# Optimization experiments

Hardware: AMD Instinct MI355X
Metric: run time of the kernel (lower is better)

The kernel has to match this reference:

```python
import jax, jax.numpy as jnp
import numpy as np

H = 4096
IN = 512
OUT = 64


def setup_inputs() -> dict:
    key = jax.random.key(0)
    ks = jax.random.split(key, 10)
    return {
        "inp": jax.random.normal(ks[0], (1, IN), jnp.float32),
        "hidden": jax.random.normal(ks[1], (1, H), jnp.float32),
        "hebb": jax.random.normal(ks[2], (H, H), jnp.float32) * 0.01,
        "W_i2h": jax.random.normal(ks[3], (H, IN), jnp.float32) * (1.0 / np.sqrt(IN)),
        "b_i2h": jax.random.normal(ks[4], (H,), jnp.float32),
        "w": jax.random.uniform(ks[5], (H, H), jnp.float32) * 0.01,
        "plas": jax.random.uniform(ks[6], (H, H), jnp.float32) * 0.01,
        "learn": jnp.full((1,), 0.01, jnp.float32),
        "W_h2o": jax.random.normal(ks[7], (OUT, H), jnp.float32) * (1.0 / np.sqrt(H)),
        "b_h2o": jax.random.normal(ks[8], (OUT,), jnp.float32),
    }


def reference(inp, hidden, hebb, W_i2h, b_i2h, w, plas, learn, W_h2o, b_h2o):
    # plastic-Miconi, rule='hebb', activ='relu'
    # x = relu(i2h(input) + hidden @ (w + plas * hebb))   [1, H]
    pre = inp @ W_i2h.T + b_i2h + hidden @ (w + plas * hebb)
    x = jax.nn.relu(pre)
    # hebb <- (1 - learn) * hebb + learn * outer(hidden, x)   [H, H]
    hebb_new = (1.0 - learn) * hebb + learn * (hidden.T @ x)
    # output = tanh(h2o(x))   [1, OUT]
    out = jnp.tanh(x @ W_h2o.T + b_h2o)
    return out, x, hebb_new
```

## Files before the change

kernel.cpp:

```cpp
#include <hip/hip_runtime.h>
#include <math.h>

#define H 4096
#define INP 512
#define OUTN 64
#define H4 (H / 4)
#define SPLITS 512
#define RPS (H / SPLITS)

typedef float fx4 __attribute__((ext_vector_type(4)));

__global__ __launch_bounds__(256) void k_partial(
    const float* __restrict__ hidden,
    const float* __restrict__ w,
    const float* __restrict__ plas,
    const float* __restrict__ hebb,
    float* __restrict__ partial)
{
    const int col4 = blockIdx.x * 256 + threadIdx.x;
    const int i0   = blockIdx.y * RPS;
    const fx4* __restrict__ w4 = (const fx4*)w;
    const fx4* __restrict__ p4 = (const fx4*)plas;
    const fx4* __restrict__ h4 = (const fx4*)hebb;

    fx4 acc = (fx4)(0.f);
    size_t idx = (size_t)i0 * H4 + col4;
#pragma unroll
    for (int r = 0; r < RPS; r += 2) {
        const float hv0 = hidden[i0 + r];
        const float hv1 = hidden[i0 + r + 1];
        const fx4 wv0 = __builtin_nontemporal_load(w4 + idx);
        const fx4 pv0 = __builtin_nontemporal_load(p4 + idx);
        const fx4 hb0 = h4[idx];
        const fx4 wv1 = __builtin_nontemporal_load(w4 + idx + H4);
        const fx4 pv1 = __builtin_nontemporal_load(p4 + idx + H4);
        const fx4 hb1 = h4[idx + H4];
        acc += hv0 * (wv0 + pv0 * hb0) + hv1 * (wv1 + pv1 * hb1);
        idx += 2 * (size_t)H4;
    }
    ((fx4*)partial)[(size_t)blockIdx.y * H4 + col4] = acc;
}

__global__ __launch_bounds__(256) void k_reduce_x(
    const float* __restrict__ partial,
    const float* __restrict__ inp,
    const float* __restrict__ W_i2h,
    const float* __restrict__ b_i2h,
    float* __restrict__ x_out)
{
    const int jl  = threadIdx.x & 31;
    const int grp = threadIdx.x >> 5;
    const int j   = blockIdx.x * 32 + jl;

    float sum = 0.f;
    const float* __restrict__ p = partial + (size_t)grp * 64 * H + j;
#pragma unroll 8
    for (int s = 0; s < 64; ++s)
        sum += p[(size_t)s * H];

    const fx4* __restrict__ row4 = (const fx4*)(W_i2h + (size_t)j * INP);
    const fx4* __restrict__ in4  = (const fx4*)inp;
#pragma unroll
    for (int c = 0; c < 16; ++c) {
        const fx4 a = row4[grp * 16 + c];
        const fx4 b = in4[grp * 16 + c];
        sum += a.x * b.x + a.y * b.y + a.z * b.z + a.w * b.w;
    }

    __shared__ float red[8][32];
    red[grp][jl] = sum;
    __syncthreads();
    if (threadIdx.x < 32) {
        float t = 0.f;
#pragma unroll
        for (int g = 0; g < 8; ++g) t += red[g][jl];
        const float pre = t + b_i2h[j];
        x_out[j] = pre > 0.f ? pre : 0.f;
    }
}

__global__ __launch_bounds__(256) void k_hebb(
    const float* __restrict__ hebb,
    const float* __restrict__ hidden,
    const float* __restrict__ x,
    const float* __restrict__ learn,
    float* __restrict__ hebb_out)
{
    const int i = blockIdx.x;
    const float lr   = learn[0];
    const float om   = 1.f - lr;
    const float coef = lr * hidden[i];
    const fx4* __restrict__ hb4 = (const fx4*)hebb + (size_t)i * H4;
    const fx4* __restrict__ xx4 = (const fx4*)x;
    fx4* __restrict__ o4 = (fx4*)hebb_out + (size_t)i * H4;

    const int t = threadIdx.x;
    const fx4 a0 = hb4[t];
    const fx4 a1 = hb4[t + 256];
    const fx4 a2 = hb4[t + 512];
    const fx4 a3 = hb4[t + 768];
    const fx4 x0 = xx4[t];
    const fx4 x1 = xx4[t + 256];
    const fx4 x2 = xx4[t + 512];
    const fx4 x3 = xx4[t + 768];
    __builtin_nontemporal_store(om * a0 + coef * x0, o4 + t);
    __builtin_nontemporal_store(om * a1 + coef * x1, o4 + t + 256);
    __builtin_nontemporal_store(om * a2 + coef * x2, o4 + t + 512);
    __builtin_nontemporal_store(om * a3 + coef * x3, o4 + t + 768);
}

__global__ __launch_bounds__(256) void k_out(
    const float* __restrict__ x,
    const float* __restrict__ W_h2o,
    const float* __restrict__ b_h2o,
    float* __restrict__ out)
{
    const int o = blockIdx.x;
    const fx4* __restrict__ row4 = (const fx4*)(W_h2o + (size_t)o * H);
    const fx4* __restrict__ x4   = (const fx4*)x;
    float sum = 0.f;
#pragma unroll
    for (int c = threadIdx.x; c < H4; c += 256) {
        const fx4 a = row4[c];
        const fx4 b = x4[c];
        sum += a.x * b.x + a.y * b.y + a.z * b.z + a.w * b.w;
    }
#pragma unroll
    for (int off = 32; off > 0; off >>= 1)
        sum += __shfl_down(sum, off, 64);
    __shared__ float red[4];
    const int lane = threadIdx.x & 63;
    const int wave = threadIdx.x >> 6;
    if (lane == 0) red[wave] = sum;
    __syncthreads();
    if (threadIdx.x == 0) {
        const float s = red[0] + red[1] + red[2] + red[3];
        out[o] = tanhf(s + b_h2o[o]);
    }
}

extern "C" void kernel_launch(void* const* d_in, const int* in_sizes, int n_in,
                              void* d_out, int out_size, void* d_ws, size_t ws_size,
                              hipStream_t stream)
{
    const float* inp    = (const float*)d_in[0];
    const float* hidden = (const float*)d_in[1];
    const float* hebb   = (const float*)d_in[2];
    const float* W_i2h  = (const float*)d_in[3];
    const float* b_i2h  = (const float*)d_in[4];
    const float* w      = (const float*)d_in[5];
    const float* plas   = (const float*)d_in[6];
    const float* learn  = (const float*)d_in[7];
    const float* W_h2o  = (const float*)d_in[8];
    const float* b_h2o  = (const float*)d_in[9];

    float* out      = (float*)d_out;
    float* x        = out + OUTN;
    float* hebb_out = x + H;

    const size_t part_bytes = (size_t)SPLITS * H * sizeof(float);
    float* partial = (ws_size >= part_bytes) ? (float*)d_ws : hebb_out;

    k_partial<<<dim3(H4 / 256, SPLITS), 256, 0, stream>>>(hidden, w, plas, hebb, partial);
    k_reduce_x<<<H / 32, 256, 0, stream>>>(partial, inp, W_i2h, b_i2h, x);
    k_hebb<<<H, 256, 0, stream>>>(hebb, hidden, x, learn, hebb_out);
    k_out<<<OUTN, 256, 0, stream>>>(x, W_h2o, b_h2o, out);
}
```

Before: 245.8 us.

## Batch partial-sum loads, widen reduce block, fuse hebb update with output kernel

k_partial now issues all eight rows of hebb, w and plas loads up front before the FMA chain, which raises memory-level parallelism at the cost of more registers. k_reduce_x uses 1024-thread blocks (32 groups) so each thread reduces fewer partials, with a padded shared array. The hebb update and the h2o output kernels are merged into one launch, removing a kernel boundary, and the hebb read in the update is made nontemporal.

```diff
diff --git a/kernel.cpp b/kernel.cpp
--- a/kernel.cpp
+++ b/kernel.cpp
@@ -22,26 +22,28 @@
     const fx4* __restrict__ w4 = (const fx4*)w;
     const fx4* __restrict__ p4 = (const fx4*)plas;
     const fx4* __restrict__ h4 = (const fx4*)hebb;
+    const size_t base = (size_t)i0 * H4 + col4;
+
+    fx4 hb[RPS], wv[RPS], pv[RPS];
+#pragma unroll
+    for (int r = 0; r < RPS; ++r)
+        hb[r] = h4[base + (size_t)r * H4];
+#pragma unroll
+    for (int r = 0; r < RPS; ++r)
+        wv[r] = __builtin_nontemporal_load(w4 + base + (size_t)r * H4);
+#pragma unroll
+    for (int r = 0; r < RPS; ++r)
+        pv[r] = __builtin_nontemporal_load(p4 + base + (size_t)r * H4);
 
     fx4 acc = (fx4)(0.f);
-    size_t idx = (size_t)i0 * H4 + col4;
 #pragma unroll
-    for (int r = 0; r < RPS; r += 2) {
-        const float hv0 = hidden[i0 + r];
-        const float hv1 = hidden[i0 + r + 1];
-        const fx4 wv0 = __builtin_nontemporal_load(w4 + idx);
-        const fx4 pv0 = __builtin_nontemporal_load(p4 + idx);
-        const fx4 hb0 = h4[idx];
-        const fx4 wv1 = __builtin_nontemporal_load(w4 + idx + H4);
-        const fx4 pv1 = __builtin_nontemporal_load(p4 + idx + H4);
-        const fx4 hb1 = h4[idx + H4];
-        acc += hv0 * (wv0 + pv0 * hb0) + hv1 * (wv1 + pv1 * hb1);
-        idx += 2 * (size_t)H4;
-    }
+    for (int r = 0; r < RPS; ++r)
+        acc += hidden[i0 + r] * (wv[r] + pv[r] * hb[r]);
+
     ((fx4*)partial)[(size_t)blockIdx.y * H4 + col4] = acc;
 }
 
-__global__ __launch_bounds__(256) void k_reduce_x(
+__global__ __launch_bounds__(1024) void k_reduce_x(
     const float* __restrict__ partial,
     const float* __restrict__ inp,
     const float* __restrict__ W_i2h,
@@ -53,89 +55,87 @@
     const int j   = blockIdx.x * 32 + jl;
 
     float sum = 0.f;
-    const float* __restrict__ p = partial + (size_t)grp * 64 * H + j;
-#pragma unroll 8
-    for (int s = 0; s < 64; ++s)
+    const float* __restrict__ p = partial + (size_t)grp * (SPLITS / 32) * H + j;
+#pragma unroll
+    for (int s = 0; s < SPLITS / 32; ++s)
         sum += p[(size_t)s * H];
 
     const fx4* __restrict__ row4 = (const fx4*)(W_i2h + (size_t)j * INP);
     const fx4* __restrict__ in4  = (const fx4*)inp;
 #pragma unroll
-    for (int c = 0; c < 16; ++c) {
-        const fx4 a = row4[grp * 16 + c];
-        const fx4 b = in4[grp * 16 + c];
+    for (int c = 0; c < 4; ++c) {
+        const fx4 a = row4[grp * 4 + c];
+        const fx4 b = in4[grp * 4 + c];
         sum += a.x * b.x + a.y * b.y + a.z * b.z + a.w * b.w;
     }
 
-    __shared__ float red[8][32];
+    __shared__ float red[32][33];
     red[grp][jl] = sum;
     __syncthreads();
     if (threadIdx.x < 32) {
         float t = 0.f;
 #pragma unroll
-        for (int g = 0; g < 8; ++g) t += red[g][jl];
+        for (int g = 0; g < 32; ++g) t += red[g][jl];
         const float pre = t + b_i2h[j];
         x_out[j] = pre > 0.f ? pre : 0.f;
     }
 }
 
-__global__ __launch_bounds__(256) void k_hebb(
+__global__ __launch_bounds__(256) void k_tail(
     const float* __restrict__ hebb,
     const float* __restrict__ hidden,
     const float* __restrict__ x,
     const float* __restrict__ learn,
-    float* __restrict__ hebb_out)
-{
-    const int i = blockIdx.x;
-    const float lr   = learn[0];
-    const float om   = 1.f - lr;
-    const float coef = lr * hidden[i];
-    const fx4* __restrict__ hb4 = (const fx4*)hebb + (size_t)i * H4;
-    const fx4* __restrict__ xx4 = (const fx4*)x;
-    fx4* __restrict__ o4 = (fx4*)hebb_out + (size_t)i * H4;
-
-    const int t = threadIdx.x;
-    const fx4 a0 = hb4[t];
-    const fx4 a1 = hb4[t + 256];
-    const fx4 a2 = hb4[t + 512];
-    const fx4 a3 = hb4[t + 768];
-    const fx4 x0 = xx4[t];
-    const fx4 x1 = xx4[t + 256];
-    const fx4 x2 = xx4[t + 512];
-    const fx4 x3 = xx4[t + 768];
-    __builtin_nontemporal_store(om * a0 + coef * x0, o4 + t);
-    __builtin_nontemporal_store(om * a1 + coef * x1, o4 + t + 256);
-    __builtin_nontemporal_store(om * a2 + coef * x2, o4 + t + 512);
-    __builtin_nontemporal_store(om * a3 + coef * x3, o4 + t + 768);
-}
-
-__global__ __launch_bounds__(256) void k_out(
-    const float* __restrict__ x,
     const float* __restrict__ W_h2o,
     const float* __restrict__ b_h2o,
+    float* __restrict__ hebb_out,
     float* __restrict__ out)
 {
-    const int o = blockIdx.x;
-    const fx4* __restrict__ row4 = (const fx4*)(W_h2o + (size_t)o * H);
-    const fx4* __restrict__ x4   = (const fx4*)x;
-    float sum = 0.f;
+    if (blockIdx.x < H) {
+        const int i = blockIdx.x;
+        const float lr   = learn[0];
+        const float om   = 1.f - lr;
+        const float coef = lr * hidden[i];
+        const fx4* __restrict__ hb4 = (const fx4*)hebb + (size_t)i * H4;
+        const fx4* __restrict__ xx4 = (const fx4*)x;
+        fx4* __restrict__ o4 = (fx4*)hebb_out + (size_t)i * H4;
+
+        const int t = threadIdx.x;
+        const fx4 a0 = __builtin_nontemporal_load(hb4 + t);
+        const fx4 a1 = __builtin_nontemporal_load(hb4 + t + 256);
+        const fx4 a2 = __builtin_nontemporal_load(hb4 + t + 512);
+        const fx4 a3 = __builtin_nontemporal_load(hb4 + t + 768);
+        const fx4 x0 = xx4[t];
+        const fx4 x1 = xx4[t + 256];
+        const fx4 x2 = xx4[t + 512];
+        const fx4 x3 = xx4[t + 768];
+        __builtin_nontemporal_store(om * a0 + coef * x0, o4 + t);
+        __builtin_nontemporal_store(om * a1 + coef * x1, o4 + t + 256);
+        __builtin_nontemporal_store(om * a2 + coef * x2, o4 + t + 512);
+        __builtin_nontemporal_store(om * a3 + coef * x3, o4 + t + 768);
+    } else {
+        const int o = blockIdx.x - H;
+        const fx4* __restrict__ row4 = (const fx4*)(W_h2o + (size_t)o * H);
+        const fx4* __restrict__ x4   = (const fx4*)x;
+        float sum = 0.f;
 #pragma unroll
-    for (int c = threadIdx.x; c < H4; c += 256) {
-        const fx4 a = row4[c];
-        const fx4 b = x4[c];
-        sum += a.x * b.x + a.y * b.y + a.z * b.z + a.w * b.w;
-    }
+        for (int c = threadIdx.x; c < H4; c += 256) {
+            const fx4 a = row4[c];
+            const fx4 b = x4[c];
+            sum += a.x * b.x + a.y * b.y + a.z * b.z + a.w * b.w;
+        }
 #pragma unroll
-    for (int off = 32; off > 0; off >>= 1)
-        sum += __shfl_down(sum, off, 64);
-    __shared__ float red[4];
-    const int lane = threadIdx.x & 63;
-    const int wave = threadIdx.x >> 6;
-    if (lane == 0) red[wave] = sum;
-    __syncthreads();
-    if (threadIdx.x == 0) {
-        const float s = red[0] + red[1] + red[2] + red[3];
-        out[o] = tanhf(s + b_h2o[o]);
+        for (int off = 32; off > 0; off >>= 1)
+            sum += __shfl_down(sum, off, 64);
+        __shared__ float red[4];
+        const int lane = threadIdx.x & 63;
+        const int wave = threadIdx.x >> 6;
+        if (lane == 0) red[wave] = sum;
+        __syncthreads();
+        if (threadIdx.x == 0) {
+            const float s = red[0] + red[1] + red[2] + red[3];
+            out[o] = tanhf(s + b_h2o[o]);
+        }
     }
 }
 
@@ -162,7 +162,6 @@
     float* partial = (ws_size >= part_bytes) ? (float*)d_ws : hebb_out;
 
     k_partial<<<dim3(H4 / 256, SPLITS), 256, 0, stream>>>(hidden, w, plas, hebb, partial);
-    k_reduce_x<<<H / 32, 256, 0, stream>>>(partial, inp, W_i2h, b_i2h, x);
-    k_hebb<<<H, 256, 0, stream>>>(hebb, hidden, x, learn, hebb_out);
-    k_out<<<OUTN, 256, 0, stream>>>(x, W_h2o, b_h2o, out);
+    k_reduce_x<<<H / 32, 1024, 0, stream>>>(partial, inp, W_i2h, b_i2h, x);
+    k_tail<<<H + OUTN, 256, 0, stream>>>(hebb, hidden, x, learn, W_h2o, b_h2o, hebb_out, out);
 }
```

Measured after the change: 241.6 us. About the same (-1.7%).
